# Kernel tuning notes

Measured on AMD Instinct MI355X. Metric: run time of the kernel, lower is better.

## Reference

```python
import jax, jax.numpy as jnp
import numpy as np

N, T, K, R, DK = 4096, 8, 4, 8, 64
S = 2   # slot_dim (2D coords)
B = 20  # noise samples (hardcoded in original forward)


def _conv1d(x, w, b, pad):
    # x: [batch, Cin, L], w: [Cout, Cin, ks] (torch Conv1d layout == OIH)
    y = jax.lax.conv_general_dilated(x, w, (1,), [(pad, pad)],
                                     dimension_numbers=('NCH', 'OIH', 'NCH'))
    return y + b[None, :, None]


def setup_inputs() -> dict:
    key = jax.random.key(0)
    ks = iter(jax.random.split(key, 40))
    r = lambda shape, s=0.1: jax.random.normal(next(ks), shape, jnp.float32) * s
    return dict(
        obs=r((1, S, N, T), 1.0),
        obs_vel=r((1, S, N, T), 1.0),
        noise=r((B, 2, 1, 1), 1.0),
        wq_rule=r((S * T, DK)), bq_rule=r((DK,)),
        wq_ctx=r((2 * S * T, DK)), bq_ctx=r((DK,)),
        wk_ctx=r((2 * S * T, DK)), bk_ctx=r((DK,)),
        rule_emb=r((R, DK), 1.0),
        w_noise=r((R,), 1.0), w_indiv=r((R,), 1.0), w_social=r((R,), 1.0),
        sp_w=r((R, S, S * (K + 1), 3)), sp_b=r((R, S)),
        spr_w=r((R, S, S * (K + 1), 1)), spr_b=r((R, S)),
        tp_w=r((R, 12, T, 3)), tp_b=r((R, 12)),
        tpr_w=r((R, 12, T, 1)), tpr_b=r((R, 12)),
        spi_w=r((R, S, S, 3)), spi_b=r((R, S)),
        spir_w=r((R, S, S, 1)), spir_b=r((R, S)),
        tpi_w=r((R, 12, T, 3)), tpi_b=r((R, 12)),
        tpir_w=r((R, 12, T, 1)), tpir_b=r((R, 12)),
    )


def reference(obs, obs_vel, noise, wq_rule, bq_rule, wq_ctx, bq_ctx, wk_ctx, bk_ctx,
              rule_emb, w_noise, w_indiv, w_social,
              sp_w, sp_b, spr_w, spr_b, tp_w, tp_b, tpr_w, tpr_b,
              spi_w, spi_b, spir_w, spir_b, tpi_w, tpi_b, tpir_w, tpir_b):
    # ---- context selection (eval path: topk_onehot) ----
    cat = jnp.concatenate([obs, obs_vel], axis=1)[0]           # [2S, N, T]
    x_ctx = jnp.transpose(cat, (1, 2, 0)).reshape(N, -1)       # [N, T*2S]
    q = x_ctx @ wq_ctx + bq_ctx
    k_ = x_ctx @ wk_ctx + bk_ctx
    attn_ctx = jax.nn.softmax(q @ k_.T, axis=-1)               # [N, N]
    _, ctx_idx = jax.lax.top_k(attn_ctx, K)                    # [N, K]
    # gather == bmm with one-hot [N,N] masks in the original
    ov_node = jnp.transpose(obs_vel[0], (1, 0, 2))             # [N, S, T]
    ctx_vel = ov_node[ctx_idx]                                 # [N, K, S, T]
    ctx_vel = jnp.transpose(ctx_vel, (1, 2, 0, 3)).reshape(1, K * S, N, T)

    # ---- rule selection (hard top-1) ----
    x_rule = jnp.transpose(obs_vel[0], (1, 2, 0)).reshape(N, -1)  # [N, T*S]
    rq = x_rule @ wq_rule + bq_rule
    attn_rule = jax.nn.softmax(rq @ rule_emb.T, axis=-1)       # [N, R]
    rule_mask = jax.nn.one_hot(jnp.argmax(attn_rule, -1), R, dtype=obs.dtype)  # [N, R]

    noise_rep = jnp.tile(noise, (1, K, 1, 1))                  # [B, K*S, 1, 1]

    def rule_fn(wn, wi, ws, p):
        ov = obs_vel + noise * wn                              # [B, S, N, T]
        ov_f = jnp.transpose(ov, (0, 2, 1, 3)).reshape(B * N, S, T)
        cv = ctx_vel + noise_rep * wn                          # [B, K*S, N, T]
        cv_f = jnp.transpose(cv, (0, 2, 1, 3)).reshape(B * N, K * S, T)
        comb = jnp.concatenate([ov_f, cv_f], axis=1)           # [B*N, S*(K+1), T]
        si = jax.nn.relu(_conv1d(ov_f, p['spi_w'], p['spi_b'], 1)) \
             + _conv1d(ov_f, p['spir_w'], p['spir_b'], 0)      # [B*N, S, T]
        ti = jnp.transpose(si, (0, 2, 1))                      # [B*N, T, S]
        indiv = _conv1d(ti, p['tpi_w'], p['tpi_b'], 1) + _conv1d(ti, p['tpir_w'], p['tpir_b'], 0)
        ss = jax.nn.relu(_conv1d(comb, p['sp_w'], p['sp_b'], 1)) \
             + _conv1d(comb, p['spr_w'], p['spr_b'], 0)        # [B*N, S, T]
        ts = jnp.transpose(ss, (0, 2, 1))
        social = _conv1d(ts, p['tp_w'], p['tp_b'], 1) + _conv1d(ts, p['tpr_w'], p['tpr_b'], 0)
        return wi * indiv + ws * social                        # [B*N, 12, S]

    params = dict(sp_w=sp_w, sp_b=sp_b, spr_w=spr_w, spr_b=spr_b,
                  tp_w=tp_w, tp_b=tp_b, tpr_w=tpr_w, tpr_b=tpr_b,
                  spi_w=spi_w, spi_b=spi_b, spir_w=spir_w, spir_b=spir_b,
                  tpi_w=tpi_w, tpi_b=tpi_b, tpir_w=tpir_w, tpir_b=tpir_b)
    preds = jax.vmap(rule_fn)(w_noise, w_indiv, w_social, params)  # [R, B*N, 12, S]
    preds = preds.reshape(R, B, N, 12, S)
    # hard rule dispatch + final permute(0,2,3,1) of the original -> [B, N, 12, S]
    return jnp.einsum('rbnts,nr->bnts', preds, rule_mask)
```

## Files before the change

### kernel.cpp

```cpp
#include <hip/hip_runtime.h>
#include <cstdint>
#include <cstddef>

#define N_   4096
#define T_   8
#define K_   4
#define R_   8
#define DK_  64
#define S_   2
#define B_   20
#define NT_  (N_*T_)

__device__ __forceinline__ unsigned long long mkkey(float v, int col) {
    unsigned u = __float_as_uint(v);
    u = (u & 0x80000000u) ? ~u : (u | 0x80000000u);
    return ((unsigned long long)u << 32) | (unsigned)(~col);
}

#define INS4(t0,t1,t2,t3,keyexpr) do {                                  \
    unsigned long long _k = (keyexpr);                                  \
    if (_k > (t3)) {                                                    \
        bool _g2 = _k > (t2), _g1 = _k > (t1), _g0 = _k > (t0);         \
        (t3) = _g2 ? (t2) : _k;                                         \
        (t2) = _g2 ? (_g1 ? (t1) : _k) : (t2);                          \
        (t1) = _g1 ? (_g0 ? (t0) : _k) : (t1);                          \
        (t0) = _g0 ? _k : (t0);                                         \
    }                                                                   \
} while (0)

__device__ __forceinline__ unsigned long long shfl_xor_u64(unsigned long long v, int m) {
    unsigned lo = (unsigned)v, hi = (unsigned)(v >> 32);
    lo = __shfl_xor(lo, m, 64);
    hi = __shfl_xor(hi, m, 64);
    return ((unsigned long long)hi << 32) | lo;
}

__global__ __launch_bounds__(256) void proj_kernel(
    const float* __restrict__ obs, const float* __restrict__ obsv,
    const float* __restrict__ wq_ctx, const float* __restrict__ bq_ctx,
    const float* __restrict__ wk_ctx, const float* __restrict__ bk_ctx,
    const float* __restrict__ wq_rule, const float* __restrict__ bq_rule,
    const float* __restrict__ rule_emb,
    float* __restrict__ qg, float* __restrict__ kg, int* __restrict__ rid)
{
    int wv = threadIdx.x >> 6, d = threadIdx.x & 63;
    int n = blockIdx.x * 4 + wv;
    __shared__ float xs[4][32];
    if (d < 32) {
        int t = d >> 2, c = d & 3;
        const float* src = (c < 2) ? obs : obsv;
        xs[wv][d] = src[(c & 1) * NT_ + n * T_ + t];
    }
    __syncthreads();
    const float* x = xs[wv];
    float q = bq_ctx[d], k = bk_ctx[d], rq = bq_rule[d];
    #pragma unroll
    for (int i = 0; i < 32; ++i) {
        float xv = x[i];
        q = fmaf(xv, wq_ctx[i*64 + d], q);
        k = fmaf(xv, wk_ctx[i*64 + d], k);
    }
    #pragma unroll
    for (int i = 0; i < 16; ++i) {
        int t = i >> 1, s = i & 1;
        rq = fmaf(x[t*4 + 2 + s], wq_rule[i*64 + d], rq);
    }
    qg[n*64 + d] = q;
    kg[n*64 + d] = k;

    float best = -1e30f; int bestr = 0;
    #pragma unroll
    for (int r = 0; r < 8; ++r) {
        float p = rq * rule_emb[r*64 + d];
        #pragma unroll
        for (int off = 32; off > 0; off >>= 1) p += __shfl_xor(p, off, 64);
        if (p > best) { best = p; bestr = r; }
    }
    if (d == 0) rid[n] = bestr;
}

#define RPB     128
#define CTILE   128
#define NSPLIT  16
#define QST     64
#define KST2    128

__global__ __launch_bounds__(512) void attn_topk_kernel(
    const float* __restrict__ qg, const float* __restrict__ kg,
    unsigned long long* __restrict__ part)
{
    __shared__ float qT[DK_*RPB];
    __shared__ float kT[DK_*KST2];

    int tid = threadIdx.x;
    int tx = tid & 15, ty = tid >> 4;
    int rowblk = blockIdx.x >> 4, split = blockIdx.x & 15;
    int row0 = rowblk * RPB;
    int colbase = split * (N_ / NSPLIT);

    #pragma unroll
    for (int i = 0; i < 4; ++i) {
        int chunk = tid + 512*i;
        int row = chunk & 127, dc = chunk >> 7;
        float4 v = *(const float4*)(qg + (size_t)(row0 + row)*64 + 4*dc);
        qT[(4*dc+0)*RPB + row] = v.x;
        qT[(4*dc+1)*RPB + row] = v.y;
        qT[(4*dc+2)*RPB + row] = v.z;
        qT[(4*dc+3)*RPB + row] = v.w;
    }

    unsigned long long T0a=0,T0b=0,T0c=0,T0d=0;
    unsigned long long T1a=0,T1b=0,T1c=0,T1d=0;
    unsigned long long T2a=0,T2b=0,T2c=0,T2d=0;
    unsigned long long T3a=0,T3b=0,T3c=0,T3d=0;

    for (int tile = 0; tile < (N_/NSPLIT)/CTILE; ++tile) {
        int c0 = colbase + tile * CTILE;
        __syncthreads();
        #pragma unroll
        for (int i = 0; i < 4; ++i) {
            int chunk = tid + 512*i;
            int col = chunk & 127, dc = chunk >> 7;
            float4 v = *(const float4*)(kg + (size_t)(c0 + col)*64 + 4*dc);
            kT[(4*dc+0)*KST2 + col] = v.x;
            kT[(4*dc+1)*KST2 + col] = v.y;
            kT[(4*dc+2)*KST2 + col] = v.z;
            kT[(4*dc+3)*KST2 + col] = v.w;
        }
        __syncthreads();

        float acc[4][8];
        #pragma unroll
        for (int i = 0; i < 4; ++i)
            #pragma unroll
            for (int j = 0; j < 8; ++j) acc[i][j] = 0.f;

        #pragma unroll 2
        for (int d = 0; d < 64; ++d) {
            float4 a  = *(const float4*)(&qT[d*RPB + 4*ty]);
            float4 b0 = *(const float4*)(&kT[d*KST2 + 4*tx]);
            float4 b1 = *(const float4*)(&kT[d*KST2 + 64 + 4*tx]);
            float av[4] = {a.x, a.y, a.z, a.w};
            float bv[8] = {b0.x, b0.y, b0.z, b0.w, b1.x, b1.y, b1.z, b1.w};
            #pragma unroll
            for (int i = 0; i < 4; ++i)
                #pragma unroll
                for (int j = 0; j < 8; ++j)
                    acc[i][j] = fmaf(av[i], bv[j], acc[i][j]);
        }
        int ccA = c0 + 4*tx, ccB = c0 + 64 + 4*tx;
        #define ROW8(t0,t1,t2,t3,i) do {                         \
            INS4(t0,t1,t2,t3, mkkey(acc[i][0], ccA+0));          \
            INS4(t0,t1,t2,t3, mkkey(acc[i][1], ccA+1));          \
            INS4(t0,t1,t2,t3, mkkey(acc[i][2], ccA+2));          \
            INS4(t0,t1,t2,t3, mkkey(acc[i][3], ccA+3));          \
            INS4(t0,t1,t2,t3, mkkey(acc[i][4], ccB+0));          \
            INS4(t0,t1,t2,t3, mkkey(acc[i][5], ccB+1));          \
            INS4(t0,t1,t2,t3, mkkey(acc[i][6], ccB+2));          \
            INS4(t0,t1,t2,t3, mkkey(acc[i][7], ccB+3));          \
        } while (0)
        ROW8(T0a,T0b,T0c,T0d, 0);
        ROW8(T1a,T1b,T1c,T1d, 1);
        ROW8(T2a,T2b,T2c,T2d, 2);
        ROW8(T3a,T3b,T3c,T3d, 3);
        #undef ROW8
    }

    #pragma unroll
    for (int m = 1; m < 16; m <<= 1) {
        unsigned long long r0, r1, r2, r3;
        r0 = shfl_xor_u64(T0a, m); r1 = shfl_xor_u64(T0b, m);
        r2 = shfl_xor_u64(T0c, m); r3 = shfl_xor_u64(T0d, m);
        INS4(T0a,T0b,T0c,T0d, r0); INS4(T0a,T0b,T0c,T0d, r1);
        INS4(T0a,T0b,T0c,T0d, r2); INS4(T0a,T0b,T0c,T0d, r3);
        r0 = shfl_xor_u64(T1a, m); r1 = shfl_xor_u64(T1b, m);
        r2 = shfl_xor_u64(T1c, m); r3 = shfl_xor_u64(T1d, m);
        INS4(T1a,T1b,T1c,T1d, r0); INS4(T1a,T1b,T1c,T1d, r1);
        INS4(T1a,T1b,T1c,T1d, r2); INS4(T1a,T1b,T1c,T1d, r3);
        r0 = shfl_xor_u64(T2a, m); r1 = shfl_xor_u64(T2b, m);
        r2 = shfl_xor_u64(T2c, m); r3 = shfl_xor_u64(T2d, m);
        INS4(T2a,T2b,T2c,T2d, r0); INS4(T2a,T2b,T2c,T2d, r1);
        INS4(T2a,T2b,T2c,T2d, r2); INS4(T2a,T2b,T2c,T2d, r3);
        r0 = shfl_xor_u64(T3a, m); r1 = shfl_xor_u64(T3b, m);
        r2 = shfl_xor_u64(T3c, m); r3 = shfl_xor_u64(T3d, m);
        INS4(T3a,T3b,T3c,T3d, r0); INS4(T3a,T3b,T3c,T3d, r1);
        INS4(T3a,T3b,T3c,T3d, r2); INS4(T3a,T3b,T3c,T3d, r3);
    }

    if (tx == 0) {
        unsigned long long* q;
        q = &part[(size_t)((row0 + 4*ty + 0)*NSPLIT + split)*4];
        q[0]=T0a; q[1]=T0b; q[2]=T0c; q[3]=T0d;
        q = &part[(size_t)((row0 + 4*ty + 1)*NSPLIT + split)*4];
        q[0]=T1a; q[1]=T1b; q[2]=T1c; q[3]=T1d;
        q = &part[(size_t)((row0 + 4*ty + 2)*NSPLIT + split)*4];
        q[0]=T2a; q[1]=T2b; q[2]=T2c; q[3]=T2d;
        q = &part[(size_t)((row0 + 4*ty + 3)*NSPLIT + split)*4];
        q[0]=T3a; q[1]=T3b; q[2]=T3c; q[3]=T3d;
    }
}

__global__ __launch_bounds__(256) void merge_kernel(
    const unsigned long long* __restrict__ part, int* __restrict__ cidx)
{
    int n = blockIdx.x * blockDim.x + threadIdx.x;
    if (n >= N_) return;
    unsigned long long m0=0,m1=0,m2=0,m3=0;
    #pragma unroll 8
    for (int j = 0; j < NSPLIT*4; ++j) INS4(m0,m1,m2,m3, part[(size_t)n*NSPLIT*4 + j]);
    cidx[n*4 + 0] = (int)(~((unsigned)(m0 & 0xffffffffull)));
    cidx[n*4 + 1] = (int)(~((unsigned)(m1 & 0xffffffffull)));
    cidx[n*4 + 2] = (int)(~((unsigned)(m2 & 0xffffffffull)));
    cidx[n*4 + 3] = (int)(~((unsigned)(m3 & 0xffffffffull)));
}

#define WST 708

__global__ __launch_bounds__(256) void prep_kernel(
    const float* __restrict__ sp_w, const float* __restrict__ sp_b,
    const float* __restrict__ spr_w, const float* __restrict__ spr_b,
    const float* __restrict__ tp_w, const float* __restrict__ tp_b,
    const float* __restrict__ tpr_w, const float* __restrict__ tpr_b,
    const float* __restrict__ spi_w, const float* __restrict__ spi_b,
    const float* __restrict__ spir_w, const float* __restrict__ spir_b,
    const float* __restrict__ tpi_w, const float* __restrict__ tpi_b,
    const float* __restrict__ tpir_w, const float* __restrict__ tpir_b,
    float* __restrict__ Wpk)
{
    int r = blockIdx.x;
    for (int o = threadIdx.x; o < 704; o += 256) {
        float v;
        if (o < 12)      v = spi_w[r*12 + o];
        else if (o < 16) v = spir_w[r*4 + (o-12)];
        else if (o < 76) v = sp_w[r*60 + (o-16)];
        else if (o < 96) v = spr_w[r*20 + (o-76)];
        else if (o < 192) { int q=o-96;  int t=q/12, co=q%12; v = tpi_w[((r*12+co)*8+t)*3+1] + tpir_w[(r*12+co)*8+t]; }
        else if (o < 288) { int q=o-192; int t=q/12, co=q%12; v = tpi_w[((r*12+co)*8+t)*3+2]; }
        else if (o < 384) { int q=o-288; int t=q/12, co=q%12; v = tpi_w[((r*12+co)*8+t)*3+0]; }
        else if (o < 480) { int q=o-384; int t=q/12, co=q%12; v = tp_w[((r*12+co)*8+t)*3+1] + tpr_w[(r*12+co)*8+t]; }
        else if (o < 576) { int q=o-480; int t=q/12, co=q%12; v = tp_w[((r*12+co)*8+t)*3+2]; }
        else if (o < 672) { int q=o-576; int t=q/12, co=q%12; v = tp_w[((r*12+co)*8+t)*3+0]; }
        else if (o < 674) v = spi_b[r*2 + (o-672)];
        else if (o < 676) v = spir_b[r*2 + (o-674)];
        else if (o < 678) v = sp_b[r*2 + (o-676)];
        else if (o < 680) v = spr_b[r*2 + (o-678)];
        else if (o < 692) v = tpi_b[r*12 + (o-680)] + tpir_b[r*12 + (o-680)];
        else              v = tp_b[r*12 + (o-692)] + tpr_b[r*12 + (o-692)];
        Wpk[r*WST + o] = v;
    }
}

__global__ __launch_bounds__(256) void predict_kernel(
    const float* __restrict__ obsv, const float* __restrict__ noise,
    const float* __restrict__ w_noise, const float* __restrict__ w_indiv,
    const float* __restrict__ w_social,
    const float* __restrict__ Wpk,
    const int* __restrict__ rid, const int* __restrict__ cidx,
    float* __restrict__ out)
{
    __shared__ __align__(16) float W[R_*WST];
    __shared__ float nz_s[B_*2];
    __shared__ float wn_s[R_], wi_s[R_], ws_s[R_];
    int tid = threadIdx.x;

    {
        const float4* src = (const float4*)Wpk;
        float4* dst = (float4*)W;
        for (int i = tid; i < (R_*WST)/4; i += 256) dst[i] = src[i];
    }
    if (tid < B_*2)                  nz_s[tid] = noise[tid];
    if (tid >= 64  && tid < 64+R_)   wn_s[tid-64]  = w_noise[tid-64];
    if (tid >= 96  && tid < 96+R_)   wi_s[tid-96]  = w_indiv[tid-96];
    if (tid >= 128 && tid < 128+R_)  ws_s[tid-128] = w_social[tid-128];
    __syncthreads();

    int item = blockIdx.x*256 + tid;
    if (item >= B_*N_) return;
    int n = item / B_, b = item - n*B_;
    int r = rid[n];
    const float* Wr = &W[r*WST];
    float wn = wn_s[r];
    float nz0 = nz_s[b*2+0]*wn, nz1 = nz_s[b*2+1]*wn;

    float x[10][8];
    #pragma unroll
    for (int s = 0; s < 2; ++s) {
        float4 a = *(const float4*)(obsv + s*NT_ + n*8);
        float4 c = *(const float4*)(obsv + s*NT_ + n*8 + 4);
        float nz = s ? nz1 : nz0;
        x[s][0]=a.x+nz; x[s][1]=a.y+nz; x[s][2]=a.z+nz; x[s][3]=a.w+nz;
        x[s][4]=c.x+nz; x[s][5]=c.y+nz; x[s][6]=c.z+nz; x[s][7]=c.w+nz;
    }
    #pragma unroll
    for (int k = 0; k < 4; ++k) {
        int cn = cidx[n*4 + k];
        #pragma unroll
        for (int s = 0; s < 2; ++s) {
            float4 a = *(const float4*)(obsv + s*NT_ + cn*8);
            float4 c = *(const float4*)(obsv + s*NT_ + cn*8 + 4);
            float nz = s ? nz1 : nz0;
            int ch = 2 + k*2 + s;
            x[ch][0]=a.x+nz; x[ch][1]=a.y+nz; x[ch][2]=a.z+nz; x[ch][3]=a.w+nz;
            x[ch][4]=c.x+nz; x[ch][5]=c.y+nz; x[ch][6]=c.z+nz; x[ch][7]=c.w+nz;
        }
    }

    float si[2][8];
    #pragma unroll
    for (int so = 0; so < 2; ++so) {
        float pre[8];
        float bb = Wr[672+so];
        #pragma unroll
        for (int t = 0; t < 8; ++t) pre[t] = bb;
        #pragma unroll
        for (int ci = 0; ci < 2; ++ci) {
            float w0 = Wr[so*6+ci*3+0], w1 = Wr[so*6+ci*3+1], w2 = Wr[so*6+ci*3+2];
            pre[0] += x[ci][0]*w1 + x[ci][1]*w2;
            #pragma unroll
            for (int t = 1; t < 7; ++t) pre[t] += x[ci][t-1]*w0 + x[ci][t]*w1 + x[ci][t+1]*w2;
            pre[7] += x[ci][6]*w0 + x[ci][7]*w1;
        }
        float l0 = Wr[12+so*2+0], l1 = Wr[12+so*2+1];
        float lb = Wr[674+so];
        #pragma unroll
        for (int t = 0; t < 8; ++t)
            si[so][t] = fmaxf(pre[t], 0.f) + lb + x[0][t]*l0 + x[1][t]*l1;
    }

    float ss[2][8];
    #pragma unroll
    for (int so = 0; so < 2; ++so) {
        float pre[8], lin[8];
        float bb = Wr[676+so], lb = Wr[678+so];
        #pragma unroll
        for (int t = 0; t < 8; ++t) { pre[t] = bb; lin[t] = lb; }
        #pragma unroll
        for (int ci = 0; ci < 10; ++ci) {
            float w0 = Wr[16+so*30+ci*3+0], w1 = Wr[16+so*30+ci*3+1], w2 = Wr[16+so*30+ci*3+2];
            float lw = Wr[76+so*10+ci];
            pre[0] += x[ci][0]*w1 + x[ci][1]*w2;
            #pragma unroll
            for (int t = 1; t < 7; ++t) pre[t] += x[ci][t-1]*w0 + x[ci][t]*w1 + x[ci][t+1]*w2;
            pre[7] += x[ci][6]*w0 + x[ci][7]*w1;
            #pragma unroll
            for (int t = 0; t < 8; ++t) lin[t] += x[ci][t]*lw;
        }
        #pragma unroll
        for (int t = 0; t < 8; ++t) ss[so][t] = fmaxf(pre[t], 0.f) + lin[t];
    }

    float i0[12], i1[12], s0a[12], s1a[12];
    #pragma unroll
    for (int g = 0; g < 3; ++g) {
        float4 bi = *(const float4*)(&Wr[680 + g*4]);
        float4 bs = *(const float4*)(&Wr[692 + g*4]);
        i0[g*4+0]=bi.x; i0[g*4+1]=bi.y; i0[g*4+2]=bi.z; i0[g*4+3]=bi.w;
        i1[g*4+0]=bi.x; i1[g*4+1]=bi.y; i1[g*4+2]=bi.z; i1[g*4+3]=bi.w;
        s0a[g*4+0]=bs.x; s0a[g*4+1]=bs.y; s0a[g*4+2]=bs.z; s0a[g*4+3]=bs.w;
        s1a[g*4+0]=bs.x; s1a[g*4+1]=bs.y; s1a[g*4+2]=bs.z; s1a[g*4+3]=bs.w;
    }
    #pragma unroll
    for (int t = 0; t < 8; ++t) {
        float a0 = si[0][t], a1 = si[1][t];
        float b0v = ss[0][t], b1v = ss[1][t];
        #pragma unroll
        for (int g = 0; g < 3; ++g) {
            float4 tA = *(const float4*)(&Wr[96  + t*12 + g*4]);
            float4 tB = *(const float4*)(&Wr[192 + t*12 + g*4]);
            float4 tC = *(const float4*)(&Wr[288 + t*12 + g*4]);
            float4 tD = *(const float4*)(&Wr[384 + t*12 + g*4]);
            float4 tE = *(const float4*)(&Wr[480 + t*12 + g*4]);
            float4 tF = *(const float4*)(&Wr[576 + t*12 + g*4]);
            #define UPD(co, C) do {                              \
                i0[co]  += a0*tA.C + a1*tB.C;                    \
                i1[co]  += a1*tA.C + a0*tC.C;                    \
                s0a[co] += b0v*tD.C + b1v*tE.C;                  \
                s1a[co] += b1v*tD.C + b0v*tF.C;                  \
            } while (0)
            UPD(g*4+0, x); UPD(g*4+1, y); UPD(g*4+2, z); UPD(g*4+3, w);
            #undef UPD
        }
    }

    float wi = wi_s[r], wsoc = ws_s[r];
    float o[24];
    #pragma unroll
    for (int co = 0; co < 12; ++co) {
        o[co*2+0] = wi*i0[co] + wsoc*s0a[co];
        o[co*2+1] = wi*i1[co] + wsoc*s1a[co];
    }
    float* dst = out + (size_t)(b*N_ + n)*24;
    #pragma unroll
    for (int q4 = 0; q4 < 6; ++q4)
        *(float4*)(dst + q4*4) = *(const float4*)(&o[q4*4]);
}

extern "C" void kernel_launch(void* const* d_in, const int* in_sizes, int n_in,
                              void* d_out, int out_size, void* d_ws, size_t ws_size,
                              hipStream_t stream)
{
    const float* obs      = (const float*)d_in[0];
    const float* obsv     = (const float*)d_in[1];
    const float* noise    = (const float*)d_in[2];
    const float* wq_rule  = (const float*)d_in[3];
    const float* bq_rule  = (const float*)d_in[4];
    const float* wq_ctx   = (const float*)d_in[5];
    const float* bq_ctx   = (const float*)d_in[6];
    const float* wk_ctx   = (const float*)d_in[7];
    const float* bk_ctx   = (const float*)d_in[8];
    const float* rule_emb = (const float*)d_in[9];
    const float* w_noise  = (const float*)d_in[10];
    const float* w_indiv  = (const float*)d_in[11];
    const float* w_social = (const float*)d_in[12];
    const float* sp_w  = (const float*)d_in[13];
    const float* sp_b  = (const float*)d_in[14];
    const float* spr_w = (const float*)d_in[15];
    const float* spr_b = (const float*)d_in[16];
    const float* tp_w  = (const float*)d_in[17];
    const float* tp_b  = (const float*)d_in[18];
    const float* tpr_w = (const float*)d_in[19];
    const float* tpr_b = (const float*)d_in[20];
    const float* spi_w  = (const float*)d_in[21];
    const float* spi_b  = (const float*)d_in[22];
    const float* spir_w = (const float*)d_in[23];
    const float* spir_b = (const float*)d_in[24];
    const float* tpi_w  = (const float*)d_in[25];
    const float* tpi_b  = (const float*)d_in[26];
    const float* tpir_w = (const float*)d_in[27];
    const float* tpir_b = (const float*)d_in[28];

    char* ws = (char*)d_ws;
    float* qg = (float*)(ws);
    float* kg = (float*)(ws + 1048576);
    unsigned long long* part = (unsigned long long*)(ws + 2097152);
    int* rid   = (int*)(ws + 4194304);
    int* cidx  = (int*)(ws + 4210688);
    float* Wpk = (float*)(ws + 4276224);

    hipLaunchKernelGGL(prep_kernel, dim3(R_), dim3(256), 0, stream,
        sp_w, sp_b, spr_w, spr_b, tp_w, tp_b, tpr_w, tpr_b,
        spi_w, spi_b, spir_w, spir_b, tpi_w, tpi_b, tpir_w, tpir_b, Wpk);

    hipLaunchKernelGGL(proj_kernel, dim3(N_/4), dim3(256), 0, stream,
        obs, obsv, wq_ctx, bq_ctx, wk_ctx, bk_ctx, wq_rule, bq_rule, rule_emb,
        qg, kg, rid);

    hipLaunchKernelGGL(attn_topk_kernel, dim3((N_/RPB)*NSPLIT), dim3(512), 0, stream,
        qg, kg, part);

    hipLaunchKernelGGL(merge_kernel, dim3(N_/256), dim3(256), 0, stream,
        part, cidx);

    hipLaunchKernelGGL(predict_kernel, dim3((B_*N_)/256), dim3(256), 0, stream,
        obsv, noise, w_noise, w_indiv, w_social, Wpk,
        rid, cidx, (float*)d_out);
}
```

Measured before the change: 205.1 us.

## Fuse prep into projection kernel and top-k merge into predict kernel

The weight-packing prep kernel becomes extra blocks of the projection kernel, and the top-k merge moves into the predict kernel. Predict now uses 320-thread blocks that cover 16 nodes with 20 samples each, and 16 threads per block reduce the partial top-k lists into shared memory. This cuts the launch count from five to three and removes the cidx round trip through global memory. In exchange, the merge runs serially on a few threads while the rest of the block waits at the barrier, and the block shape changes occupancy.

```diff
diff --git a/kernel.cpp b/kernel.cpp
--- a/kernel.cpp
+++ b/kernel.cpp
@@ -35,14 +35,50 @@
     return ((unsigned long long)hi << 32) | lo;
 }
 
-__global__ __launch_bounds__(256) void proj_kernel(
+#define WST 708
+
+__global__ __launch_bounds__(256) void proj_prep_kernel(
     const float* __restrict__ obs, const float* __restrict__ obsv,
     const float* __restrict__ wq_ctx, const float* __restrict__ bq_ctx,
     const float* __restrict__ wk_ctx, const float* __restrict__ bk_ctx,
     const float* __restrict__ wq_rule, const float* __restrict__ bq_rule,
     const float* __restrict__ rule_emb,
-    float* __restrict__ qg, float* __restrict__ kg, int* __restrict__ rid)
+    const float* __restrict__ sp_w, const float* __restrict__ sp_b,
+    const float* __restrict__ spr_w, const float* __restrict__ spr_b,
+    const float* __restrict__ tp_w, const float* __restrict__ tp_b,
+    const float* __restrict__ tpr_w, const float* __restrict__ tpr_b,
+    const float* __restrict__ spi_w, const float* __restrict__ spi_b,
+    const float* __restrict__ spir_w, const float* __restrict__ spir_b,
+    const float* __restrict__ tpi_w, const float* __restrict__ tpi_b,
+    const float* __restrict__ tpir_w, const float* __restrict__ tpir_b,
+    float* __restrict__ qg, float* __restrict__ kg, int* __restrict__ rid,
+    float* __restrict__ Wpk)
 {
+    if (blockIdx.x >= N_/4) {
+        int r = blockIdx.x - N_/4;
+        for (int o = threadIdx.x; o < 704; o += 256) {
+            float v;
+            if (o < 12)      v = spi_w[r*12 + o];
+            else if (o < 16) v = spir_w[r*4 + (o-12)];
+            else if (o < 76) v = sp_w[r*60 + (o-16)];
+            else if (o < 96) v = spr_w[r*20 + (o-76)];
+            else if (o < 192) { int q=o-96;  int t=q/12, co=q%12; v = tpi_w[((r*12+co)*8+t)*3+1] + tpir_w[(r*12+co)*8+t]; }
+            else if (o < 288) { int q=o-192; int t=q/12, co=q%12; v = tpi_w[((r*12+co)*8+t)*3+2]; }
+            else if (o < 384) { int q=o-288; int t=q/12, co=q%12; v = tpi_w[((r*12+co)*8+t)*3+0]; }
+            else if (o < 480) { int q=o-384; int t=q/12, co=q%12; v = tp_w[((r*12+co)*8+t)*3+1] + tpr_w[(r*12+co)*8+t]; }
+            else if (o < 576) { int q=o-480; int t=q/12, co=q%12; v = tp_w[((r*12+co)*8+t)*3+2]; }
+            else if (o < 672) { int q=o-576; int t=q/12, co=q%12; v = tp_w[((r*12+co)*8+t)*3+0]; }
+            else if (o < 674) v = spi_b[r*2 + (o-672)];
+            else if (o < 676) v = spir_b[r*2 + (o-674)];
+            else if (o < 678) v = sp_b[r*2 + (o-676)];
+            else if (o < 680) v = spr_b[r*2 + (o-678)];
+            else if (o < 692) v = tpi_b[r*12 + (o-680)] + tpir_b[r*12 + (o-680)];
+            else              v = tp_b[r*12 + (o-692)] + tpr_b[r*12 + (o-692)];
+            Wpk[r*WST + o] = v;
+        }
+        return;
+    }
+
     int wv = threadIdx.x >> 6, d = threadIdx.x & 63;
     int n = blockIdx.x * 4 + wv;
     __shared__ float xs[4][32];
@@ -82,7 +118,6 @@
 #define RPB     128
 #define CTILE   128
 #define NSPLIT  16
-#define QST     64
 #define KST2    128
 
 __global__ __launch_bounds__(512) void attn_topk_kernel(
@@ -200,83 +235,46 @@
     }
 }
 
-__global__ __launch_bounds__(256) void merge_kernel(
-    const unsigned long long* __restrict__ part, int* __restrict__ cidx)
-{
-    int n = blockIdx.x * blockDim.x + threadIdx.x;
-    if (n >= N_) return;
-    unsigned long long m0=0,m1=0,m2=0,m3=0;
-    #pragma unroll 8
-    for (int j = 0; j < NSPLIT*4; ++j) INS4(m0,m1,m2,m3, part[(size_t)n*NSPLIT*4 + j]);
-    cidx[n*4 + 0] = (int)(~((unsigned)(m0 & 0xffffffffull)));
-    cidx[n*4 + 1] = (int)(~((unsigned)(m1 & 0xffffffffull)));
-    cidx[n*4 + 2] = (int)(~((unsigned)(m2 & 0xffffffffull)));
-    cidx[n*4 + 3] = (int)(~((unsigned)(m3 & 0xffffffffull)));
-}
-
-#define WST 708
-
-__global__ __launch_bounds__(256) void prep_kernel(
-    const float* __restrict__ sp_w, const float* __restrict__ sp_b,
-    const float* __restrict__ spr_w, const float* __restrict__ spr_b,
-    const float* __restrict__ tp_w, const float* __restrict__ tp_b,
-    const float* __restrict__ tpr_w, const float* __restrict__ tpr_b,
-    const float* __restrict__ spi_w, const float* __restrict__ spi_b,
-    const float* __restrict__ spir_w, const float* __restrict__ spir_b,
-    const float* __restrict__ tpi_w, const float* __restrict__ tpi_b,
-    const float* __restrict__ tpir_w, const float* __restrict__ tpir_b,
-    float* __restrict__ Wpk)
-{
-    int r = blockIdx.x;
-    for (int o = threadIdx.x; o < 704; o += 256) {
-        float v;
-        if (o < 12)      v = spi_w[r*12 + o];
-        else if (o < 16) v = spir_w[r*4 + (o-12)];
-        else if (o < 76) v = sp_w[r*60 + (o-16)];
-        else if (o < 96) v = spr_w[r*20 + (o-76)];
-        else if (o < 192) { int q=o-96;  int t=q/12, co=q%12; v = tpi_w[((r*12+co)*8+t)*3+1] + tpir_w[(r*12+co)*8+t]; }
-        else if (o < 288) { int q=o-192; int t=q/12, co=q%12; v = tpi_w[((r*12+co)*8+t)*3+2]; }
-        else if (o < 384) { int q=o-288; int t=q/12, co=q%12; v = tpi_w[((r*12+co)*8+t)*3+0]; }
-        else if (o < 480) { int q=o-384; int t=q/12, co=q%12; v = tp_w[((r*12+co)*8+t)*3+1] + tpr_w[(r*12+co)*8+t]; }
-        else if (o < 576) { int q=o-480; int t=q/12, co=q%12; v = tp_w[((r*12+co)*8+t)*3+2]; }
-        else if (o < 672) { int q=o-576; int t=q/12, co=q%12; v = tp_w[((r*12+co)*8+t)*3+0]; }
-        else if (o < 674) v = spi_b[r*2 + (o-672)];
-        else if (o < 676) v = spir_b[r*2 + (o-674)];
-        else if (o < 678) v = sp_b[r*2 + (o-676)];
-        else if (o < 680) v = spr_b[r*2 + (o-678)];
-        else if (o < 692) v = tpi_b[r*12 + (o-680)] + tpir_b[r*12 + (o-680)];
-        else              v = tp_b[r*12 + (o-692)] + tpr_b[r*12 + (o-692)];
-        Wpk[r*WST + o] = v;
-    }
-}
-
-__global__ __launch_bounds__(256) void predict_kernel(
+__global__ __launch_bounds__(320) void predict_kernel(
     const float* __restrict__ obsv, const float* __restrict__ noise,
     const float* __restrict__ w_noise, const float* __restrict__ w_indiv,
     const float* __restrict__ w_social,
     const float* __restrict__ Wpk,
-    const int* __restrict__ rid, const int* __restrict__ cidx,
+    const int* __restrict__ rid, const unsigned long long* __restrict__ part,
     float* __restrict__ out)
 {
     __shared__ __align__(16) float W[R_*WST];
+    __shared__ int   cidx_s[16][4];
     __shared__ float nz_s[B_*2];
     __shared__ float wn_s[R_], wi_s[R_], ws_s[R_];
     int tid = threadIdx.x;
+    int n0 = blockIdx.x * 16;
 
     {
         const float4* src = (const float4*)Wpk;
         float4* dst = (float4*)W;
-        for (int i = tid; i < (R_*WST)/4; i += 256) dst[i] = src[i];
+        for (int i = tid; i < (R_*WST)/4; i += 320) dst[i] = src[i];
     }
     if (tid < B_*2)                  nz_s[tid] = noise[tid];
     if (tid >= 64  && tid < 64+R_)   wn_s[tid-64]  = w_noise[tid-64];
     if (tid >= 96  && tid < 96+R_)   wi_s[tid-96]  = w_indiv[tid-96];
     if (tid >= 128 && tid < 128+R_)  ws_s[tid-128] = w_social[tid-128];
+
+    if (tid >= 160 && tid < 176) {
+        int n = n0 + (tid - 160);
+        unsigned long long m0=0,m1=0,m2=0,m3=0;
+        const unsigned long long* p = &part[(size_t)n*NSPLIT*4];
+        #pragma unroll 8
+        for (int j = 0; j < NSPLIT*4; ++j) INS4(m0,m1,m2,m3, p[j]);
+        cidx_s[tid-160][0] = (int)(~((unsigned)(m0 & 0xffffffffull)));
+        cidx_s[tid-160][1] = (int)(~((unsigned)(m1 & 0xffffffffull)));
+        cidx_s[tid-160][2] = (int)(~((unsigned)(m2 & 0xffffffffull)));
+        cidx_s[tid-160][3] = (int)(~((unsigned)(m3 & 0xffffffffull)));
+    }
     __syncthreads();
 
-    int item = blockIdx.x*256 + tid;
-    if (item >= B_*N_) return;
-    int n = item / B_, b = item - n*B_;
+    int n_local = tid / 20, b = tid - n_local * 20;
+    int n = n0 + n_local;
     int r = rid[n];
     const float* Wr = &W[r*WST];
     float wn = wn_s[r];
@@ -293,7 +291,7 @@
     }
     #pragma unroll
     for (int k = 0; k < 4; ++k) {
-        int cn = cidx[n*4 + k];
+        int cn = cidx_s[n_local][k];
         #pragma unroll
         for (int s = 0; s < 2; ++s) {
             float4 a = *(const float4*)(obsv + s*NT_ + cn*8);
@@ -434,24 +432,18 @@
     float* kg = (float*)(ws + 1048576);
     unsigned long long* part = (unsigned long long*)(ws + 2097152);
     int* rid   = (int*)(ws + 4194304);
-    int* cidx  = (int*)(ws + 4210688);
-    float* Wpk = (float*)(ws + 4276224);
-
-    hipLaunchKernelGGL(prep_kernel, dim3(R_), dim3(256), 0, stream,
+    float* Wpk = (float*)(ws + 4210688);
+
+    hipLaunchKernelGGL(proj_prep_kernel, dim3(N_/4 + R_), dim3(256), 0, stream,
+        obs, obsv, wq_ctx, bq_ctx, wk_ctx, bk_ctx, wq_rule, bq_rule, rule_emb,
         sp_w, sp_b, spr_w, spr_b, tp_w, tp_b, tpr_w, tpr_b,
-        spi_w, spi_b, spir_w, spir_b, tpi_w, tpi_b, tpir_w, tpir_b, Wpk);
-
-    hipLaunchKernelGGL(proj_kernel, dim3(N_/4), dim3(256), 0, stream,
-        obs, obsv, wq_ctx, bq_ctx, wk_ctx, bk_ctx, wq_rule, bq_rule, rule_emb,
-        qg, kg, rid);
+        spi_w, spi_b, spir_w, spir_b, tpi_w, tpi_b, tpir_w, tpir_b,
+        qg, kg, rid, Wpk);
 
     hipLaunchKernelGGL(attn_topk_kernel, dim3((N_/RPB)*NSPLIT), dim3(512), 0, stream,
         qg, kg, part);
 
-    hipLaunchKernelGGL(merge_kernel, dim3(N_/256), dim3(256), 0, stream,
-        part, cidx);
-
-    hipLaunchKernelGGL(predict_kernel, dim3((B_*N_)/256), dim3(256), 0, stream,
+    hipLaunchKernelGGL(predict_kernel, dim3(N_/16), dim3(320), 0, stream,
         obsv, noise, w_noise, w_indiv, w_social, Wpk,
-        rid, cidx, (float*)d_out);
-}
+        rid, part, (float*)d_out);
+}
```

New measurement: 196.7 us. -4.1%, faster.
